# Kernel optimization log

Measured on AMD Instinct MI355X. Metric: run time of the kernel, lower is better.

## Reference

```python
import jax, jax.numpy as jnp
import numpy as np

NUM_CAPSULE = 16
DIM_CAPSULE = 64
ROUTINGS = 4
SEQ_LEN, BATCH, HIDDEN = 512, 64, 1024  # hidden = 2*num_hiddens (bidirectional)


def squash(x, axis=-1):
    s = jnp.sum(x * x, axis=axis, keepdims=True)
    return x / jnp.sqrt(s + 1e-7)


def setup_inputs() -> dict:
    key = jax.random.key(0)
    k1, k2 = jax.random.split(key)
    inputs = jax.random.normal(k1, (SEQ_LEN, BATCH, HIDDEN), dtype=jnp.float32)
    # xavier-normal std = sqrt(2/(fan_in+fan_out)) = sqrt(2/(1024+1024))
    std = float(np.sqrt(2.0 / (HIDDEN + NUM_CAPSULE * DIM_CAPSULE)))
    W = jax.random.normal(k2, (1, HIDDEN, NUM_CAPSULE * DIM_CAPSULE), dtype=jnp.float32) * std
    return {"inputs": inputs, "W": W}


def reference(inputs, W):
    # inputs: (S, B, H) -> (B, S, H)
    x = jnp.transpose(inputs, (1, 0, 2))
    B, S, H = x.shape
    # projection: (B,S,H) @ (H, nc*dc) -> (B,S,nc*dc)
    u = jnp.einsum('bsh,ho->bso', x, W[0])
    u = u.reshape(B, S, NUM_CAPSULE, DIM_CAPSULE)
    u = jnp.transpose(u, (0, 2, 1, 3))  # (B, nc, S, dc)
    b = jnp.zeros((B, NUM_CAPSULE, S, 1), dtype=x.dtype)
    outputs = None
    for i in range(ROUTINGS):
        c = jax.nn.softmax(b, axis=1)  # softmax over capsules
        outputs = squash(jnp.sum(c * u, axis=2))  # (B, nc, dc)
        if i < ROUTINGS - 1:
            update = jnp.sum(outputs[:, :, None, :] * u, axis=-1, keepdims=True)
            b = b + update
    return outputs
```

## Files before the change

kernel.cpp:

```cpp
#include <hip/hip_runtime.h>

typedef unsigned short u16;
typedef __attribute__((ext_vector_type(4))) float f32x4;
typedef __attribute__((ext_vector_type(8))) unsigned short u16x8;
typedef __attribute__((ext_vector_type(4))) unsigned short u16x4;
typedef __attribute__((ext_vector_type(8))) short s16x8;

__device__ __forceinline__ u16 f2bf(float f) {
    unsigned u = __float_as_uint(f);
    u += 0x7FFFu + ((u >> 16) & 1u);
    return (u16)(u >> 16);
}
__device__ __forceinline__ float bf2f(u16 h) {
    return __uint_as_float(((unsigned)h) << 16);
}

__global__ void wtrans_k(const float* __restrict__ W, u16* __restrict__ Wt) {
    __shared__ float tile[32][33];
    const int k0 = blockIdx.x << 5, n0 = blockIdx.y << 5;
    const int tx = threadIdx.x & 31, ty = threadIdx.x >> 5;
#pragma unroll
    for (int r = 0; r < 32; r += 8)
        tile[ty + r][tx] = W[(size_t)(k0 + ty + r) * 1024 + n0 + tx];
    __syncthreads();
#pragma unroll
    for (int r = 0; r < 32; r += 8)
        Wt[(size_t)(n0 + ty + r) * 1024 + k0 + tx] = f2bf(tile[tx][ty + r]);
}

__global__ void gemm_k(const float* __restrict__ X, const u16* __restrict__ Wt,
                       u16* __restrict__ U) {
    __shared__ u16 lds[16384];
    const int tid = threadIdx.x;
    const int lane = tid & 63, wave = tid >> 6;
    const int bid = blockIdx.x;
    const int tm = bid >> 3, tn = bid & 7;
    const int r0 = tm << 7, c0 = tn << 7;
    const int wm = wave >> 1, wn = wave & 1;

    const int arow = tid >> 1, ahalf = tid & 1;
    const int s_ = (r0 + arow) & 511, b_ = (r0 + arow) >> 9;
    const float* asrc = X + ((size_t)s_ * 64 + b_) * 1024 + (ahalf << 4);
    const u16* bsrc = Wt + ((size_t)(c0 + arow)) * 1024 + (ahalf << 4);
    const int sOff = (arow << 5) + (ahalf << 4);

    const int lrow = lane & 15, lk = (lane >> 4) << 3;

    f32x4 acc[4][4] = {};

    {
        const f32x4* ap = (const f32x4*)asrc;
        f32x4 A0 = ap[0], A1 = ap[1], A2 = ap[2], A3 = ap[3];
        const u16x8* bp = (const u16x8*)bsrc;
        u16x8 B0 = bp[0], B1 = bp[1];
        u16x8 pa0, pa1;
#pragma unroll
        for (int j = 0; j < 4; ++j) {
            pa0[j] = f2bf(A0[j]); pa0[4 + j] = f2bf(A1[j]);
            pa1[j] = f2bf(A2[j]); pa1[4 + j] = f2bf(A3[j]);
        }
        *(u16x8*)&lds[sOff] = pa0;       *(u16x8*)&lds[sOff + 8] = pa1;
        *(u16x8*)&lds[8192 + sOff] = B0; *(u16x8*)&lds[8192 + sOff + 8] = B1;
    }
    __syncthreads();

#pragma unroll 2
    for (int kt = 0; kt < 32; ++kt) {
        const int cur = kt & 1, nxt = cur ^ 1;
        f32x4 A0, A1, A2, A3;
        u16x8 B0, B1;
        const bool has_next = (kt < 31);
        if (has_next) {
            const int k0 = (kt + 1) << 5;
            const f32x4* ap = (const f32x4*)(asrc + k0);
            A0 = ap[0]; A1 = ap[1]; A2 = ap[2]; A3 = ap[3];
            const u16x8* bp = (const u16x8*)(bsrc + k0);
            B0 = bp[0]; B1 = bp[1];
        }
        const u16* sA = lds + cur * 4096;
        const u16* sB = lds + 8192 + cur * 4096;
        s16x8 af[4], bfr[4];
#pragma unroll
        for (int m = 0; m < 4; ++m)
            af[m] = *(const s16x8*)&sA[((wm << 6) + (m << 4) + lrow) * 32 + lk];
#pragma unroll
        for (int n = 0; n < 4; ++n)
            bfr[n] = *(const s16x8*)&sB[((wn << 6) + (n << 4) + lrow) * 32 + lk];
#pragma unroll
        for (int m = 0; m < 4; ++m)
#pragma unroll
            for (int n = 0; n < 4; ++n)
                acc[m][n] = __builtin_amdgcn_mfma_f32_16x16x32_bf16(af[m], bfr[n], acc[m][n], 0, 0, 0);
        if (has_next) {
            u16x8 pa0, pa1;
#pragma unroll
            for (int j = 0; j < 4; ++j) {
                pa0[j] = f2bf(A0[j]); pa0[4 + j] = f2bf(A1[j]);
                pa1[j] = f2bf(A2[j]); pa1[4 + j] = f2bf(A3[j]);
            }
            u16* dA = lds + nxt * 4096;
            u16* dB = lds + 8192 + nxt * 4096;
            *(u16x8*)&dA[sOff] = pa0; *(u16x8*)&dA[sOff + 8] = pa1;
            *(u16x8*)&dB[sOff] = B0;  *(u16x8*)&dB[sOff + 8] = B1;
        }
        __syncthreads();
    }

    u16* sC = lds;
#pragma unroll
    for (int m = 0; m < 4; ++m)
#pragma unroll
        for (int n = 0; n < 4; ++n)
#pragma unroll
            for (int j = 0; j < 4; ++j) {
                const int row = (wm << 6) + (m << 4) + ((lane >> 4) << 2) + j;
                const int col = (wn << 6) + (n << 4) + (lane & 15);
                sC[(row << 7) + col] = f2bf(acc[m][n][j]);
            }
    __syncthreads();
    const int orow = tid >> 1, ocol = (tid & 1) << 6;
    u16* gdst = U + ((size_t)(r0 + orow) << 10) + c0 + ocol;
    const u16* sp = sC + (orow << 7) + ocol;
#pragma unroll
    for (int q = 0; q < 8; ++q)
        *(u16x8*)(gdst + (q << 3)) = *(const u16x8*)(sp + (q << 3));
}

__global__ void colsum_k(const u16* __restrict__ U, float* __restrict__ W0) {
    const int b = blockIdx.x, ch = blockIdx.y;
    const int t = threadIdx.x;
    const u16* base = U + (((size_t)b * 512 + ch * 64) << 10) + (t << 2);
    float a0 = 0, a1 = 0, a2 = 0, a3 = 0;
#pragma unroll 8
    for (int r = 0; r < 64; ++r) {
        u16x4 u4 = *(const u16x4*)(base + ((size_t)r << 10));
        a0 += bf2f(u4[0]); a1 += bf2f(u4[1]); a2 += bf2f(u4[2]); a3 += bf2f(u4[3]);
    }
    float* w = W0 + (b << 10) + (t << 2);
    atomicAdd(w, a0); atomicAdd(w + 1, a1); atomicAdd(w + 2, a2); atomicAdd(w + 3, a3);
}

__global__ void squash_k(const float* __restrict__ Win, float* __restrict__ Vout) {
    const int g = (blockIdx.x << 2) + (threadIdx.x >> 6);
    const int lane = threadIdx.x & 63;
    float x = Win[((size_t)g << 6) + lane];
    float s = x * x;
#pragma unroll
    for (int d = 1; d < 64; d <<= 1) s += __shfl_xor(s, d);
    Vout[((size_t)g << 6) + lane] = x / sqrtf(s + 1e-7f);
}

__global__ void route_pass(const u16* __restrict__ U, const float* __restrict__ V,
                           float* __restrict__ Bbuf, float* __restrict__ Wout,
                           const int hasB, const int writeB) {
    const int tid = threadIdx.x;
    const int wave = tid >> 6, lane = tid & 63;
    const int b = blockIdx.y;
    const int grp = lane >> 2, sub = lane & 3;
    __shared__ float wlds[1024];
    for (int q = tid; q < 1024; q += 256) wlds[q] = 0.f;
    float v[16];
    const float* vp = V + (size_t)((b << 4) + grp) * 64 + (sub << 4);
#pragma unroll
    for (int j = 0; j < 16; ++j) v[j] = vp[j];
    float wacc[16] = {};
    const int s0 = (blockIdx.x << 5) + (wave << 3);
    __syncthreads();
#pragma unroll 2
    for (int ss = 0; ss < 8; ++ss) {
        const int s = s0 + ss;
        const size_t rbase = (size_t)(b << 9) + s;
        const u16x8* up = (const u16x8*)(U + (rbase << 10) + (lane << 4));
        u16x8 u0 = up[0], u1 = up[1];
        float uf[16];
#pragma unroll
        for (int j = 0; j < 8; ++j) { uf[j] = bf2f(u0[j]); uf[8 + j] = bf2f(u1[j]); }
        float p = 0.f;
#pragma unroll
        for (int j = 0; j < 16; ++j) p = fmaf(uf[j], v[j], p);
        p += __shfl_xor(p, 1);
        p += __shfl_xor(p, 2);
        float bn = p;
        if (hasB) bn += Bbuf[(rbase << 4) + grp];
        float mx = bn;
#pragma unroll
        for (int d = 4; d < 64; d <<= 1) mx = fmaxf(mx, __shfl_xor(mx, d));
        float e = __expf(bn - mx);
        float sm = e;
#pragma unroll
        for (int d = 4; d < 64; d <<= 1) sm += __shfl_xor(sm, d);
        const float c = e / sm;
        if (writeB && sub == 0) Bbuf[(rbase << 4) + grp] = bn;
#pragma unroll
        for (int j = 0; j < 16; ++j) wacc[j] = fmaf(c, uf[j], wacc[j]);
    }
#pragma unroll
    for (int j = 0; j < 16; ++j) atomicAdd(&wlds[(lane << 4) + j], wacc[j]);
    __syncthreads();
    for (int q = tid; q < 1024; q += 256) atomicAdd(&Wout[(size_t)(b << 10) + q], wlds[q]);
}

#define WS_U   ((size_t)0)
#define WS_WT  ((size_t)67108864)
#define WS_W   ((size_t)69206016)
#define WS_V   ((size_t)70254592)
#define WS_B   ((size_t)71041024)

extern "C" void kernel_launch(void* const* d_in, const int* in_sizes, int n_in,
                              void* d_out, int out_size, void* d_ws, size_t ws_size,
                              hipStream_t stream) {
    (void)in_sizes; (void)n_in; (void)out_size; (void)ws_size;
    const float* x = (const float*)d_in[0];
    const float* W = (const float*)d_in[1];
    float* out = (float*)d_out;
    char* ws = (char*)d_ws;
    u16* U = (u16*)(ws + WS_U);
    u16* Wt = (u16*)(ws + WS_WT);
    float* wbuf = (float*)(ws + WS_W);
    float* vbuf = (float*)(ws + WS_V);
    float* bbuf = (float*)(ws + WS_B);

    hipMemsetAsync(wbuf, 0, 4 * 65536 * sizeof(float), stream);
    wtrans_k<<<dim3(32, 32), 256, 0, stream>>>(W, Wt);
    gemm_k<<<2048, 256, 0, stream>>>(x, Wt, U);
    colsum_k<<<dim3(64, 8), 256, 0, stream>>>(U, wbuf);
    squash_k<<<256, 256, 0, stream>>>(wbuf, vbuf);
    route_pass<<<dim3(16, 64), 256, 0, stream>>>(U, vbuf, bbuf, wbuf + 65536, 0, 1);
    squash_k<<<256, 256, 0, stream>>>(wbuf + 65536, vbuf + 65536);
    route_pass<<<dim3(16, 64), 256, 0, stream>>>(U, vbuf + 65536, bbuf, wbuf + 2 * 65536, 1, 1);
    squash_k<<<256, 256, 0, stream>>>(wbuf + 2 * 65536, vbuf + 2 * 65536);
    route_pass<<<dim3(16, 64), 256, 0, stream>>>(U, vbuf + 2 * 65536, bbuf, wbuf + 3 * 65536, 1, 0);
    squash_k<<<256, 256, 0, stream>>>(wbuf + 3 * 65536, out);
}
```

Measured before the change: 455.8 us.

## Fuse column-sum into GEMM, use direct global-to-LDS loads, swizzle blocks, prefetch routing

The GEMM now sums its fp32 accumulators per column and atomically adds them into the first routing buffer, which removes the separate colsum kernel that re-read U. The B operand is loaded straight into LDS with global_load_lds instead of passing through registers. The block index is swizzled so that consecutive blocks share the same column tile of Wt. The routing pass prefetches U rows in two batches of four and reduces across waves through padded LDS rather than LDS atomics. The trade-offs are more atomics inside the GEMM, a routing sum taken from unrounded fp32 values instead of the bf16 U, and changed register pressure.

```diff
diff --git a/kernel.cpp b/kernel.cpp
--- a/kernel.cpp
+++ b/kernel.cpp
@@ -3,7 +3,6 @@
 typedef unsigned short u16;
 typedef __attribute__((ext_vector_type(4))) float f32x4;
 typedef __attribute__((ext_vector_type(8))) unsigned short u16x8;
-typedef __attribute__((ext_vector_type(4))) unsigned short u16x4;
 typedef __attribute__((ext_vector_type(8))) short s16x8;
 
 __device__ __forceinline__ u16 f2bf(float f) {
@@ -14,6 +13,11 @@
 __device__ __forceinline__ float bf2f(u16 h) {
     return __uint_as_float(((unsigned)h) << 16);
 }
+__device__ __forceinline__ void gload_lds16(const void* g, void* l) {
+    __builtin_amdgcn_global_load_lds(
+        (const __attribute__((address_space(1))) unsigned int*)g,
+        (__attribute__((address_space(3))) unsigned int*)l, 16, 0, 0);
+}
 
 __global__ void wtrans_k(const float* __restrict__ W, u16* __restrict__ Wt) {
     __shared__ float tile[32][33];
@@ -29,38 +33,40 @@
 }
 
 __global__ void gemm_k(const float* __restrict__ X, const u16* __restrict__ Wt,
-                       u16* __restrict__ U) {
+                       u16* __restrict__ U, float* __restrict__ W0) {
     __shared__ u16 lds[16384];
     const int tid = threadIdx.x;
     const int lane = tid & 63, wave = tid >> 6;
-    const int bid = blockIdx.x;
-    const int tm = bid >> 3, tn = bid & 7;
+    const int swz = (int)blockIdx.x;
+    const int orig = ((swz & 7) << 8) + (swz >> 3);
+    const int tm = orig >> 3, tn = orig & 7;
     const int r0 = tm << 7, c0 = tn << 7;
     const int wm = wave >> 1, wn = wave & 1;
 
     const int arow = tid >> 1, ahalf = tid & 1;
     const int s_ = (r0 + arow) & 511, b_ = (r0 + arow) >> 9;
     const float* asrc = X + ((size_t)s_ * 64 + b_) * 1024 + (ahalf << 4);
-    const u16* bsrc = Wt + ((size_t)(c0 + arow)) * 1024 + (ahalf << 4);
     const int sOff = (arow << 5) + (ahalf << 4);
 
+    const u16* bg0 = Wt + ((size_t)(c0 + (tid >> 2)) << 10) + ((tid & 3) << 3);
+    const u16* bg1 = bg0 + (size_t)(64 << 10);
+    const int bOff = (wave << 9);
+
     const int lrow = lane & 15, lk = (lane >> 4) << 3;
-
     f32x4 acc[4][4] = {};
 
     {
         const f32x4* ap = (const f32x4*)asrc;
         f32x4 A0 = ap[0], A1 = ap[1], A2 = ap[2], A3 = ap[3];
-        const u16x8* bp = (const u16x8*)bsrc;
-        u16x8 B0 = bp[0], B1 = bp[1];
+        gload_lds16(bg0, &lds[8192 + bOff]);
+        gload_lds16(bg1, &lds[8192 + bOff + 2048]);
         u16x8 pa0, pa1;
 #pragma unroll
         for (int j = 0; j < 4; ++j) {
             pa0[j] = f2bf(A0[j]); pa0[4 + j] = f2bf(A1[j]);
             pa1[j] = f2bf(A2[j]); pa1[4 + j] = f2bf(A3[j]);
         }
-        *(u16x8*)&lds[sOff] = pa0;       *(u16x8*)&lds[sOff + 8] = pa1;
-        *(u16x8*)&lds[8192 + sOff] = B0; *(u16x8*)&lds[8192 + sOff + 8] = B1;
+        *(u16x8*)&lds[sOff] = pa0; *(u16x8*)&lds[sOff + 8] = pa1;
     }
     __syncthreads();
 
@@ -68,14 +74,13 @@
     for (int kt = 0; kt < 32; ++kt) {
         const int cur = kt & 1, nxt = cur ^ 1;
         f32x4 A0, A1, A2, A3;
-        u16x8 B0, B1;
         const bool has_next = (kt < 31);
         if (has_next) {
-            const int k0 = (kt + 1) << 5;
-            const f32x4* ap = (const f32x4*)(asrc + k0);
+            const int k0e = (kt + 1) << 5;
+            const f32x4* ap = (const f32x4*)(asrc + k0e);
             A0 = ap[0]; A1 = ap[1]; A2 = ap[2]; A3 = ap[3];
-            const u16x8* bp = (const u16x8*)(bsrc + k0);
-            B0 = bp[0]; B1 = bp[1];
+            gload_lds16(bg0 + k0e, &lds[8192 + nxt * 4096 + bOff]);
+            gload_lds16(bg1 + k0e, &lds[8192 + nxt * 4096 + bOff + 2048]);
         }
         const u16* sA = lds + cur * 4096;
         const u16* sB = lds + 8192 + cur * 4096;
@@ -99,9 +104,7 @@
                 pa1[j] = f2bf(A2[j]); pa1[4 + j] = f2bf(A3[j]);
             }
             u16* dA = lds + nxt * 4096;
-            u16* dB = lds + 8192 + nxt * 4096;
             *(u16x8*)&dA[sOff] = pa0; *(u16x8*)&dA[sOff + 8] = pa1;
-            *(u16x8*)&dB[sOff] = B0;  *(u16x8*)&dB[sOff + 8] = B1;
         }
         __syncthreads();
     }
@@ -117,6 +120,21 @@
                 const int col = (wn << 6) + (n << 4) + (lane & 15);
                 sC[(row << 7) + col] = f2bf(acc[m][n][j]);
             }
+    {
+        const int bb = tm >> 2;
+#pragma unroll
+        for (int n = 0; n < 4; ++n) {
+            float p = 0.f;
+#pragma unroll
+            for (int m = 0; m < 4; ++m)
+#pragma unroll
+                for (int j = 0; j < 4; ++j) p += acc[m][n][j];
+            p += __shfl_xor(p, 16);
+            p += __shfl_xor(p, 32);
+            if (lane < 16)
+                atomicAdd(&W0[(bb << 10) + c0 + (wn << 6) + (n << 4) + lane], p);
+        }
+    }
     __syncthreads();
     const int orow = tid >> 1, ocol = (tid & 1) << 6;
     u16* gdst = U + ((size_t)(r0 + orow) << 10) + c0 + ocol;
@@ -124,20 +142,6 @@
 #pragma unroll
     for (int q = 0; q < 8; ++q)
         *(u16x8*)(gdst + (q << 3)) = *(const u16x8*)(sp + (q << 3));
-}
-
-__global__ void colsum_k(const u16* __restrict__ U, float* __restrict__ W0) {
-    const int b = blockIdx.x, ch = blockIdx.y;
-    const int t = threadIdx.x;
-    const u16* base = U + (((size_t)b * 512 + ch * 64) << 10) + (t << 2);
-    float a0 = 0, a1 = 0, a2 = 0, a3 = 0;
-#pragma unroll 8
-    for (int r = 0; r < 64; ++r) {
-        u16x4 u4 = *(const u16x4*)(base + ((size_t)r << 10));
-        a0 += bf2f(u4[0]); a1 += bf2f(u4[1]); a2 += bf2f(u4[2]); a3 += bf2f(u4[3]);
-    }
-    float* w = W0 + (b << 10) + (t << 2);
-    atomicAdd(w, a0); atomicAdd(w + 1, a1); atomicAdd(w + 2, a2); atomicAdd(w + 3, a3);
 }
 
 __global__ void squash_k(const float* __restrict__ Win, float* __restrict__ Vout) {
@@ -155,49 +159,77 @@
                            const int hasB, const int writeB) {
     const int tid = threadIdx.x;
     const int wave = tid >> 6, lane = tid & 63;
-    const int b = blockIdx.y;
+    const int b = blockIdx.y, bx = blockIdx.x;
     const int grp = lane >> 2, sub = lane & 3;
-    __shared__ float wlds[1024];
-    for (int q = tid; q < 1024; q += 256) wlds[q] = 0.f;
+    __shared__ float wlds[4 * 64 * 20];
     float v[16];
     const float* vp = V + (size_t)((b << 4) + grp) * 64 + (sub << 4);
 #pragma unroll
     for (int j = 0; j < 16; ++j) v[j] = vp[j];
     float wacc[16] = {};
-    const int s0 = (blockIdx.x << 5) + (wave << 3);
-    __syncthreads();
-#pragma unroll 2
-    for (int ss = 0; ss < 8; ++ss) {
-        const int s = s0 + ss;
-        const size_t rbase = (size_t)(b << 9) + s;
-        const u16x8* up = (const u16x8*)(U + (rbase << 10) + (lane << 4));
-        u16x8 u0 = up[0], u1 = up[1];
-        float uf[16];
-#pragma unroll
-        for (int j = 0; j < 8; ++j) { uf[j] = bf2f(u0[j]); uf[8 + j] = bf2f(u1[j]); }
-        float p = 0.f;
-#pragma unroll
-        for (int j = 0; j < 16; ++j) p = fmaf(uf[j], v[j], p);
-        p += __shfl_xor(p, 1);
-        p += __shfl_xor(p, 2);
-        float bn = p;
-        if (hasB) bn += Bbuf[(rbase << 4) + grp];
-        float mx = bn;
-#pragma unroll
-        for (int d = 4; d < 64; d <<= 1) mx = fmaxf(mx, __shfl_xor(mx, d));
-        float e = __expf(bn - mx);
-        float sm = e;
-#pragma unroll
-        for (int d = 4; d < 64; d <<= 1) sm += __shfl_xor(sm, d);
-        const float c = e / sm;
-        if (writeB && sub == 0) Bbuf[(rbase << 4) + grp] = bn;
-#pragma unroll
-        for (int j = 0; j < 16; ++j) wacc[j] = fmaf(c, uf[j], wacc[j]);
-    }
-#pragma unroll
-    for (int j = 0; j < 16; ++j) atomicAdd(&wlds[(lane << 4) + j], wacc[j]);
-    __syncthreads();
-    for (int q = tid; q < 1024; q += 256) atomicAdd(&Wout[(size_t)(b << 10) + q], wlds[q]);
+    const int s0 = (bx << 5) + (wave << 3);
+    const size_t rbase0 = (size_t)(b << 9) + s0;
+    const u16* ubase = U + (rbase0 << 10) + (lane << 4);
+
+    u16x8 cv0[4], cv1[4], nv0[4], nv1[4];
+#pragma unroll
+    for (int r = 0; r < 4; ++r) {
+        const u16x8* up = (const u16x8*)(ubase + ((size_t)r << 10));
+        cv0[r] = up[0]; cv1[r] = up[1];
+    }
+#pragma unroll
+    for (int half = 0; half < 2; ++half) {
+        if (half == 0) {
+#pragma unroll
+            for (int r = 0; r < 4; ++r) {
+                const u16x8* up = (const u16x8*)(ubase + ((size_t)(r + 4) << 10));
+                nv0[r] = up[0]; nv1[r] = up[1];
+            }
+        }
+#pragma unroll
+        for (int r = 0; r < 4; ++r) {
+            const int s = s0 + (half << 2) + r;
+            const size_t rb = (size_t)(b << 9) + s;
+            float uf[16];
+#pragma unroll
+            for (int j = 0; j < 8; ++j) { uf[j] = bf2f(cv0[r][j]); uf[8 + j] = bf2f(cv1[r][j]); }
+            float p = 0.f;
+#pragma unroll
+            for (int j = 0; j < 16; ++j) p = fmaf(uf[j], v[j], p);
+            p += __shfl_xor(p, 1);
+            p += __shfl_xor(p, 2);
+            float bn = p;
+            if (hasB) bn += Bbuf[(rb << 4) + grp];
+            float mx = bn;
+#pragma unroll
+            for (int d = 4; d < 64; d <<= 1) mx = fmaxf(mx, __shfl_xor(mx, d));
+            float e = __expf(bn - mx);
+            float sm = e;
+#pragma unroll
+            for (int d = 4; d < 64; d <<= 1) sm += __shfl_xor(sm, d);
+            const float c = e / sm;
+            if (writeB && sub == 0) Bbuf[(rb << 4) + grp] = bn;
+#pragma unroll
+            for (int j = 0; j < 16; ++j) wacc[j] = fmaf(c, uf[j], wacc[j]);
+        }
+        if (half == 0) {
+#pragma unroll
+            for (int r = 0; r < 4; ++r) { cv0[r] = nv0[r]; cv1[r] = nv1[r]; }
+        }
+    }
+    const int rowb = ((wave << 6) + lane) * 20;
+#pragma unroll
+    for (int j = 0; j < 16; ++j) wlds[rowb + j] = wacc[j];
+    __syncthreads();
+#pragma unroll
+    for (int c = 0; c < 4; ++c) {
+        const int q = tid + (c << 8);
+        const int l = q >> 4, j = q & 15;
+        float s = 0.f;
+#pragma unroll
+        for (int w = 0; w < 4; ++w) s += wlds[((w << 6) + l) * 20 + j];
+        atomicAdd(&Wout[((size_t)b << 10) + q], s);
+    }
 }
 
 #define WS_U   ((size_t)0)
@@ -222,8 +254,7 @@
 
     hipMemsetAsync(wbuf, 0, 4 * 65536 * sizeof(float), stream);
     wtrans_k<<<dim3(32, 32), 256, 0, stream>>>(W, Wt);
-    gemm_k<<<2048, 256, 0, stream>>>(x, Wt, U);
-    colsum_k<<<dim3(64, 8), 256, 0, stream>>>(U, wbuf);
+    gemm_k<<<2048, 256, 0, stream>>>(x, Wt, U, wbuf);
     squash_k<<<256, 256, 0, stream>>>(wbuf, vbuf);
     route_pass<<<dim3(16, 64), 256, 0, stream>>>(U, vbuf, bbuf, wbuf + 65536, 0, 1);
     squash_k<<<256, 256, 0, stream>>>(wbuf + 65536, vbuf + 65536);
```

New measurement: 407.0 us. -10.7%, faster.
